# Optimization experiments

Measured on AMD Instinct MI355X. Metric: run time of the kernel, lower is better.

## Reference

```python
import jax, jax.numpy as jnp
import numpy as np

DIM = 1024
N_HEADS = 16
HEAD_DIM = DIM // N_HEADS
MAX_SEQ = 2048
BATCH = 4
SEQ = 2048


def _rope_tables(seq_len, head_dim):
    inv_freq = 1.0 / (10000.0 ** (jnp.arange(0, head_dim, 2, dtype=jnp.float32) / head_dim))
    t = jnp.arange(seq_len, dtype=jnp.float32)
    freqs = jnp.outer(t, inv_freq)            # [S, D/2]
    emb = jnp.concatenate([freqs, freqs], axis=-1)  # [S, D]
    return jnp.cos(emb), jnp.sin(emb)


def setup_inputs() -> dict:
    key = jax.random.key(0)
    kx, kq, kk, kv, ko = jax.random.split(key, 5)
    s = 1.0 / np.sqrt(DIM)
    x = jax.random.normal(kx, (BATCH, SEQ, DIM), dtype=jnp.float32)
    Wq = jax.random.normal(kq, (DIM, DIM), dtype=jnp.float32) * s
    Wk = jax.random.normal(kk, (DIM, DIM), dtype=jnp.float32) * s
    Wv = jax.random.normal(kv, (DIM, DIM), dtype=jnp.float32) * s
    Wo = jax.random.normal(ko, (DIM, DIM), dtype=jnp.float32) * s
    cos, sin = _rope_tables(SEQ, HEAD_DIM)
    mask = jnp.tril(jnp.ones((SEQ, SEQ), dtype=bool))[None, None]  # [1,1,S,S] causal
    return {"x": x, "Wq": Wq, "Wk": Wk, "Wv": Wv, "Wo": Wo,
            "cos": cos, "sin": sin, "mask": mask}


def _rotate_half(t):
    t1, t2 = jnp.split(t, 2, axis=-1)
    return jnp.concatenate([-t2, t1], axis=-1)


def reference(x, Wq, Wk, Wv, Wo, cos, sin, mask):
    B, S, _ = x.shape
    # projections (torch Linear: y = x @ W.T)
    q = (x @ Wq.T).reshape(B, S, N_HEADS, HEAD_DIM)
    k = (x @ Wk.T).reshape(B, S, N_HEADS, HEAD_DIM)
    v = (x @ Wv.T).reshape(B, S, N_HEADS, HEAD_DIM)
    # RoPE on [B,S,H,D]: cos/sin broadcast over batch and heads
    c = cos[None, :S, None, :]
    s_ = sin[None, :S, None, :]
    q = q * c + _rotate_half(q) * s_
    k = k * c + _rotate_half(k) * s_
    # attention, heads-major
    scale = HEAD_DIM ** -0.5
    attn = jnp.einsum('bqhd,bkhd->bhqk', q, k) * scale
    attn = jnp.where(mask, attn, -jnp.inf)
    attn = jax.nn.softmax(attn, axis=-1)
    out = jnp.einsum('bhqk,bkhd->bqhd', attn, v).reshape(B, S, DIM)
    return out @ Wo.T
```

## Files before the change

kernel.cpp:

```cpp
#include <hip/hip_runtime.h>
#include <hip/hip_bf16.h>
#include <stdint.h>

typedef __bf16 bf16;
typedef __bf16 bf16x4 __attribute__((ext_vector_type(4)));
typedef __bf16 bf16x8 __attribute__((ext_vector_type(8)));
typedef float f32x4 __attribute__((ext_vector_type(4)));

static constexpr int DIMM  = 1024;
static constexpr int NHEADS = 16;
static constexpr int HDIM  = 64;
static constexpr int SEQL  = 2048;
static constexpr int NB    = 4;
static constexpr int MTOT  = NB * SEQL;
static constexpr float LOG2E = 1.4426950408889634f;

__device__ __forceinline__ int swz(int row, int kc) {
    return row * 128 + ((kc ^ (row & 7)) << 4);
}

__device__ __forceinline__ void gl_lds16(const bf16* g, bf16* l) {
    __builtin_amdgcn_global_load_lds(
        (const __attribute__((address_space(1))) unsigned int*)g,
        (__attribute__((address_space(3))) unsigned int*)l,
        16, 0, 0);
}

__device__ __forceinline__ bf16x8 cvt8(f32x4 a, f32x4 b) {
    bf16x8 r;
    r[0] = (bf16)a[0]; r[1] = (bf16)a[1]; r[2] = (bf16)a[2]; r[3] = (bf16)a[3];
    r[4] = (bf16)b[0]; r[5] = (bf16)b[1]; r[6] = (bf16)b[2]; r[7] = (bf16)b[3];
    return r;
}

__global__ __launch_bounds__(256)
void cvt_kernel(const float* __restrict__ x,  const float* __restrict__ Wq,
                const float* __restrict__ Wk, const float* __restrict__ Wv,
                const float* __restrict__ Wo,
                bf16* __restrict__ xb,  bf16* __restrict__ Wqb,
                bf16* __restrict__ Wkb, bf16* __restrict__ Wvb,
                bf16* __restrict__ Wob)
{
    const size_t NX = (size_t)MTOT * DIMM;
    const size_t NW = (size_t)DIMM * DIMM;
    size_t i = ((size_t)blockIdx.x * 256 + threadIdx.x) * 8;
    const float* src; bf16* dst; size_t off;
    if (i < NX) { src = x; dst = xb; off = i; }
    else {
        size_t j = i - NX;
        int wsel = (int)(j >> 20);
        off = j & (NW - 1);
        if      (wsel == 0) { src = Wq; dst = Wqb; }
        else if (wsel == 1) { src = Wk; dst = Wkb; }
        else if (wsel == 2) { src = Wv; dst = Wvb; }
        else                { src = Wo; dst = Wob; }
    }
    f32x4 a = *(const f32x4*)(src + off);
    f32x4 b = *(const f32x4*)(src + off + 4);
    *(bf16x8*)(dst + off) = cvt8(a, b);
}

__global__ __launch_bounds__(256, 2)
void qkv_kernel(const bf16* __restrict__ xb,
                const bf16* __restrict__ Wqb, const bf16* __restrict__ Wkb,
                const bf16* __restrict__ Wvb,
                const float* __restrict__ cosT, const float* __restrict__ sinT,
                bf16* __restrict__ qb, bf16* __restrict__ kb, bf16* __restrict__ vTb)
{
    __shared__ __align__(16) bf16 As[2][128 * 32];
    __shared__ __align__(16) bf16 Bq[2][128 * 32];
    __shared__ __align__(16) bf16 Bk[2][128 * 32];
    __shared__ __align__(16) bf16 Bv[2][128 * 32];

    const int bid = (int)blockIdx.x;
    const int bn  = (bid & 7) * 128;
    const int bm  = (bid >> 3) * 128;

    const int tid  = threadIdx.x;
    const int lane = tid & 63;
    const int w    = tid >> 6;
    const int l15  = lane & 15;
    const int lg   = lane >> 4;
    const int wm   = (w >> 1) * 64;
    const int wn   = (w & 1) * 64;

    f32x4 acc[3][4][4];
    #pragma unroll
    for (int w3 = 0; w3 < 3; ++w3)
        #pragma unroll
        for (int mf = 0; mf < 4; ++mf)
            #pragma unroll
            for (int nf = 0; nf < 4; ++nf)
                acc[w3][mf][nf] = f32x4{0.f, 0.f, 0.f, 0.f};

    const int c0  = w * 2;
    const int rp0 = lane >> 3;
    const int tt  = (lane & 7) ^ rp0;
    const int rgo = (tt >> 2) << 6;
    const int kq  = (tt & 3) * 8;

    auto stage = [&](int t, int buf) {
        const int k0 = t * 32;
        #pragma unroll
        for (int i = 0; i < 2; ++i) {
            const int c  = c0 + i;
            const int rg = c * 8 + rp0 + rgo;
            const size_t am = (size_t)(bm + rg) * DIMM + k0 + kq;
            const size_t an = (size_t)(bn + rg) * DIMM + k0 + kq;
            gl_lds16(xb  + am, &As[buf][c * 512]);
            gl_lds16(Wqb + an, &Bq[buf][c * 512]);
            gl_lds16(Wkb + an, &Bk[buf][c * 512]);
            gl_lds16(Wvb + an, &Bv[buf][c * 512]);
        }
    };

    auto rd = [&](const bf16* base, int row) {
        return *(const bf16x8*)((const char*)base +
            (row & 63) * 128 + (((((row >> 6) << 2) | lg) ^ (row & 7)) << 4));
    };

    auto compute = [&](int buf) {
        bf16x8 af[4];
        #pragma unroll
        for (int mf = 0; mf < 4; ++mf)
            af[mf] = rd(As[buf], wm + mf * 16 + l15);
        const bf16* bsel[3] = {Bq[buf], Bk[buf], Bv[buf]};
        __builtin_amdgcn_s_setprio(1);
        #pragma unroll
        for (int w3 = 0; w3 < 3; ++w3) {
            bf16x8 bfr[4];
            #pragma unroll
            for (int nf = 0; nf < 4; ++nf)
                bfr[nf] = rd(bsel[w3], wn + nf * 16 + l15);
            #pragma unroll
            for (int mf = 0; mf < 4; ++mf)
                #pragma unroll
                for (int nf = 0; nf < 4; ++nf)
                    acc[w3][mf][nf] = __builtin_amdgcn_mfma_f32_16x16x32_bf16(
                        af[mf], bfr[nf], acc[w3][mf][nf], 0, 0, 0);
        }
        __builtin_amdgcn_s_setprio(0);
    };

    stage(0, 0);
    #pragma unroll 1
    for (int t = 0; t < 31; ++t) {
        stage(t + 1, (t + 1) & 1);
        asm volatile("s_waitcnt vmcnt(8)" ::: "memory");
        __builtin_amdgcn_s_barrier();
        __builtin_amdgcn_sched_barrier(0);
        compute(t & 1);
        __builtin_amdgcn_sched_barrier(0);
        __builtin_amdgcn_s_barrier();
    }
    asm volatile("s_waitcnt vmcnt(0)" ::: "memory");
    __builtin_amdgcn_s_barrier();
    __builtin_amdgcn_sched_barrier(0);
    compute(1);

    #pragma unroll
    for (int mf = 0; mf < 4; ++mf) {
        #pragma unroll
        for (int nf = 0; nf < 4; ++nf) {
            int n = bn + wn + nf * 16 + l15;
            int h = n >> 6;
            int d = n & 63;
            float sign = (d < 32) ? -1.f : 1.f;
            #pragma unroll
            for (int r = 0; r < 4; ++r) {
                int m = bm + wm + mf * 16 + lg * 4 + r;
                int b = m >> 11, s = m & 2047;
                float c  = cosT[s * 64 + d];
                float sv = sinT[s * 64 + d];
                size_t o_qk = ((size_t)((b * NHEADS + h) * SEQL + s)) * HDIM + d;
                float q0 = acc[0][mf][nf][r], q1 = acc[0][mf][nf ^ 2][r];
                float k0v = acc[1][mf][nf][r], k1 = acc[1][mf][nf ^ 2][r];
                qb[o_qk] = (bf16)((q0 * c + sign * q1 * sv) * (0.125f * LOG2E));
                kb[o_qk] = (bf16)(k0v * c + sign * k1 * sv);
                vTb[((size_t)((b * NHEADS + h) * HDIM + d)) * SEQL + s] = (bf16)acc[2][mf][nf][r];
            }
        }
    }
}

__global__ __launch_bounds__(256, 3)
void attn_kernel(bf16* __restrict__ qb, const bf16* __restrict__ kb,
                 const bf16* __restrict__ vTb)
{
    __shared__ __align__(16) bf16 Ks[2][64 * 64];
    __shared__ __align__(16) bf16 Vs[2][64 * 64];
    __shared__ __align__(16) bf16 Pl[4][32 * 64];

    const int bh  = blockIdx.x;
    const int qt  = 15 - (int)blockIdx.y;
    const int tid = threadIdx.x;
    const int lane = tid & 63, w = tid >> 6;
    const int l15 = lane & 15, lg = lane >> 4;

    bf16*       Qp = qb  + (size_t)bh * SEQL * HDIM;
    const bf16* Kp = kb  + (size_t)bh * SEQL * HDIM;
    const bf16* Vp = vTb + (size_t)bh * HDIM * SEQL;

    const int q0  = qt * 128 + w * 32;
    const int njt = 2 * qt + 2;

    bf16x8 qf[2][2];
    #pragma unroll
    for (int mf = 0; mf < 2; ++mf)
        #pragma unroll
        for (int ks = 0; ks < 2; ++ks)
            qf[mf][ks] = *(const bf16x8*)(Qp + (size_t)(q0 + mf * 16 + l15) * HDIM + ks * 32 + lg * 8);

    f32x4 oacc[4][2];
    float lsum[2] = {0.f, 0.f};
    #pragma unroll
    for (int nd = 0; nd < 4; ++nd)
        #pragma unroll
        for (int mf = 0; mf < 2; ++mf)
            oacc[nd][mf] = f32x4{0.f, 0.f, 0.f, 0.f};

    char* Pw = (char*)Pl[w];
    const int l7 = l15 & 7;
    const int srow0 = tid >> 3;
    const int skc   = tid & 7;

    bf16x8 kr[2], vr[2];
    auto issue = [&](int j) {
        const int kk0 = j * 64;
        #pragma unroll
        for (int c = 0; c < 2; ++c) {
            int row = c * 32 + srow0;
            kr[c] = *(const bf16x8*)(Kp + (size_t)(kk0 + row) * HDIM + skc * 8);
            vr[c] = *(const bf16x8*)(Vp + (size_t)row * SEQL + kk0 + skc * 8);
        }
    };
    auto commit = [&](int b) {
        #pragma unroll
        for (int c = 0; c < 2; ++c) {
            int row = c * 32 + srow0;
            *(bf16x8*)((char*)Ks[b] + swz(row, skc)) = kr[c];
            *(bf16x8*)((char*)Vs[b] + swz(row, skc)) = vr[c];
        }
    };

    issue(0);
    commit(0);
    __syncthreads();

    for (int j = 0; j < njt; ++j) {
        const int kk0 = j * 64;
        const int buf = j & 1;
        const bool more = (j + 1 < njt);
        if (more) issue(j + 1);

        f32x4 sacc[4][2];
        #pragma unroll
        for (int nf = 0; nf < 4; ++nf)
            #pragma unroll
            for (int mf = 0; mf < 2; ++mf)
                sacc[nf][mf] = f32x4{0.f, 0.f, 0.f, 0.f};
        #pragma unroll
        for (int ks = 0; ks < 2; ++ks) {
            bf16x8 kf[4];
            #pragma unroll
            for (int nf = 0; nf < 4; ++nf)
                kf[nf] = *(const bf16x8*)((const char*)Ks[buf] + swz(nf * 16 + l15, ks * 4 + lg));
            #pragma unroll
            for (int nf = 0; nf < 4; ++nf)
                #pragma unroll
                for (int mf = 0; mf < 2; ++mf)
                    sacc[nf][mf] = __builtin_amdgcn_mfma_f32_16x16x32_bf16(
                        kf[nf], qf[mf][ks], sacc[nf][mf], 0, 0, 0);
        }

        const bool nm = (kk0 + 63 > q0);
        #pragma unroll
        for (int nf = 0; nf < 4; ++nf) {
            #pragma unroll
            for (int mf = 0; mf < 2; ++mf) {
                float pv[4];
                #pragma unroll
                for (int r = 0; r < 4; ++r) {
                    float s = sacc[nf][mf][r];
                    if (nm) {
                        int kv = kk0 + nf * 16 + lg * 4 + r;
                        int qq = q0 + mf * 16 + l15;
                        if (kv > qq) s = -1.0e30f;
                    }
                    pv[r] = exp2f(s);
                }
                lsum[mf] += (pv[0] + pv[1]) + (pv[2] + pv[3]);
                bf16x4 pb;
                pb[0] = (bf16)pv[0]; pb[1] = (bf16)pv[1];
                pb[2] = (bf16)pv[2]; pb[3] = (bf16)pv[3];
                *(bf16x4*)(Pw + (mf * 16 + l15) * 128
                              + (((2 * nf + (lg >> 1)) ^ l7) << 4) + (lg & 1) * 8) = pb;
            }
        }

        #pragma unroll
        for (int ks = 0; ks < 2; ++ks) {
            bf16x8 pf[2], vf[4];
            #pragma unroll
            for (int mf = 0; mf < 2; ++mf)
                pf[mf] = *(const bf16x8*)(Pw + (mf * 16 + l15) * 128
                                             + (((ks * 4 + lg) ^ l7) << 4));
            #pragma unroll
            for (int nd = 0; nd < 4; ++nd)
                vf[nd] = *(const bf16x8*)((const char*)Vs[buf] + swz(nd * 16 + l15, ks * 4 + lg));
            #pragma unroll
            for (int nd = 0; nd < 4; ++nd)
                #pragma unroll
                for (int mf = 0; mf < 2; ++mf)
                    oacc[nd][mf] = __builtin_amdgcn_mfma_f32_16x16x32_bf16(
                        vf[nd], pf[mf], oacc[nd][mf], 0, 0, 0);
        }

        if (more) {
            commit(buf ^ 1);
            __syncthreads();
        }
    }

    #pragma unroll
    for (int mf = 0; mf < 2; ++mf) {
        lsum[mf] += __shfl_xor(lsum[mf], 16);
        lsum[mf] += __shfl_xor(lsum[mf], 32);
    }
    float inv[2] = {1.f / lsum[0], 1.f / lsum[1]};
    #pragma unroll
    for (int nd = 0; nd < 4; ++nd)
        #pragma unroll
        for (int mf = 0; mf < 2; ++mf) {
            bf16x4 o4;
            #pragma unroll
            for (int r = 0; r < 4; ++r)
                o4[r] = (bf16)(oacc[nd][mf][r] * inv[mf]);
            int s = q0 + mf * 16 + l15;
            int d = nd * 16 + lg * 4;
            *(bf16x4*)(Qp + (size_t)s * HDIM + d) = o4;
        }
}

__global__ __launch_bounds__(256, 2)
void oproj_kernel(const bf16* __restrict__ O, const bf16* __restrict__ Wob,
                  float* __restrict__ outp)
{
    __shared__ __align__(16) bf16 Bs[2][128 * 32];

    const int bm = (int)blockIdx.x * 128;
    const int bn = (int)blockIdx.y * 128;

    const int tid  = threadIdx.x;
    const int lane = tid & 63;
    const int w    = tid >> 6;
    const int l15  = lane & 15;
    const int lg   = lane >> 4;
    const int wm   = (w >> 1) * 64;
    const int wn   = (w & 1) * 64;

    f32x4 acc[4][4];
    #pragma unroll
    for (int mf = 0; mf < 4; ++mf)
        #pragma unroll
        for (int nf = 0; nf < 4; ++nf)
            acc[mf][nf] = f32x4{0.f, 0.f, 0.f, 0.f};

    const int c0  = w * 2;
    const int rp0 = lane >> 3;
    const int tt  = (lane & 7) ^ rp0;
    const int rgo = (tt >> 2) << 6;
    const int kq  = (tt & 3) * 8;

    auto stageB = [&](int t, int buf) {
        const int k0 = t * 32;
        #pragma unroll
        for (int i = 0; i < 2; ++i) {
            const int c  = c0 + i;
            const int rg = c * 8 + rp0 + rgo;
            gl_lds16(Wob + (size_t)(bn + rg) * DIMM + k0 + kq, &Bs[buf][c * 512]);
        }
    };

    auto loadA = [&](bf16x8 (&dst)[4], int t) {
        const int k0 = t * 32;
        #pragma unroll
        for (int mf = 0; mf < 4; ++mf) {
            int m = bm + wm + mf * 16 + l15;
            int b = m >> 11, s = m & 2047;
            int k = k0 + lg * 8;
            int h = k >> 6, dd = k & 63;
            dst[mf] = *(const bf16x8*)(O + ((size_t)((b * NHEADS + h) * SEQL + s)) * HDIM + dd);
        }
    };

    auto rd = [&](const bf16* base, int row) {
        return *(const bf16x8*)((const char*)base +
            (row & 63) * 128 + (((((row >> 6) << 2) | lg) ^ (row & 7)) << 4));
    };

    auto compute = [&](int buf, const bf16x8 (&af)[4]) {
        bf16x8 bfr[4];
        #pragma unroll
        for (int nf = 0; nf < 4; ++nf)
            bfr[nf] = rd(Bs[buf], wn + nf * 16 + l15);
        #pragma unroll
        for (int mf = 0; mf < 4; ++mf)
            #pragma unroll
            for (int nf = 0; nf < 4; ++nf)
                acc[mf][nf] = __builtin_amdgcn_mfma_f32_16x16x32_bf16(
                    af[mf], bfr[nf], acc[mf][nf], 0, 0, 0);
    };

    bf16x8 aA[4], aB[4];

    stageB(0, 0);
    __builtin_amdgcn_sched_barrier(0);
    loadA(aA, 0);
    __builtin_amdgcn_sched_barrier(0);

    auto step = [&](bf16x8 (&cur)[4], bf16x8 (&nxt)[4], int t) {
        stageB(t + 1, (t + 1) & 1);
        __builtin_amdgcn_sched_barrier(0);
        asm volatile("s_waitcnt vmcnt(6)" ::: "memory");
        __builtin_amdgcn_s_barrier();
        __builtin_amdgcn_sched_barrier(0);
        loadA(nxt, t + 1);
        compute(t & 1, cur);
        __builtin_amdgcn_sched_barrier(0);
        __builtin_amdgcn_s_barrier();
    };

    #pragma unroll 1
    for (int tp = 0; tp < 15; ++tp) {
        step(aA, aB, 2 * tp);
        step(aB, aA, 2 * tp + 1);
    }
    step(aA, aB, 30);
    asm volatile("s_waitcnt vmcnt(0)" ::: "memory");
    __builtin_amdgcn_s_barrier();
    __builtin_amdgcn_sched_barrier(0);
    compute(1, aB);

    #pragma unroll
    for (int mf = 0; mf < 4; ++mf)
        #pragma unroll
        for (int nf = 0; nf < 4; ++nf) {
            int n = bn + wn + nf * 16 + l15;
            #pragma unroll
            for (int r = 0; r < 4; ++r) {
                int m = bm + wm + mf * 16 + lg * 4 + r;
                outp[(size_t)m * DIMM + n] = acc[mf][nf][r];
            }
        }
}

extern "C" void kernel_launch(void* const* d_in, const int* in_sizes, int n_in,
                              void* d_out, int out_size, void* d_ws, size_t ws_size,
                              hipStream_t stream)
{
    const float* x    = (const float*)d_in[0];
    const float* Wq   = (const float*)d_in[1];
    const float* Wk   = (const float*)d_in[2];
    const float* Wv   = (const float*)d_in[3];
    const float* Wo   = (const float*)d_in[4];
    const float* cosT = (const float*)d_in[5];
    const float* sinT = (const float*)d_in[6];

    const size_t NELEM = (size_t)MTOT * DIMM;
    const size_t NW    = (size_t)DIMM * DIMM;
    bf16* qb  = (bf16*)d_ws;
    bf16* kb  = qb + NELEM;
    bf16* vT  = kb + NELEM;
    bf16* xb  = vT + NELEM;
    bf16* Wqb = xb + NELEM;
    bf16* Wkb = Wqb + NW;
    bf16* Wvb = Wkb + NW;
    bf16* Wob = Wvb + NW;

    dim3 blk(256);
    cvt_kernel<<<dim3(6144), blk, 0, stream>>>(x, Wq, Wk, Wv, Wo,
                                               xb, Wqb, Wkb, Wvb, Wob);

    qkv_kernel<<<dim3(512), blk, 0, stream>>>(xb, Wqb, Wkb, Wvb, cosT, sinT,
                                              qb, kb, vT);

    dim3 g2(NB * NHEADS, SEQL / 128);
    attn_kernel<<<g2, blk, 0, stream>>>(qb, kb, vT);

    dim3 g3(MTOT / 128, DIMM / 128);
    oproj_kernel<<<g3, blk, 0, stream>>>(qb, Wob, (float*)d_out);
}
```

Measured before the change: 176.2 us.

## Fuse x fp32-to-bf16 conversion into QKV GEMM and compute softmax row sums via MFMA

The separate conversion pass over x is removed. The QKV kernel now streams fp32 x tiles directly into LDS and converts them to bf16 when it loads fragments, which avoids writing and re-reading a bf16 copy of x. In exchange the A tile in LDS doubles in size and global reads of x in the GEMM double, which raises LDS use and may cut occupancy. Separately, the attention kernel computes the softmax denominator with an extra MFMA against a ones vector instead of scalar adds plus cross-lane shuffles, so the sum is now taken over bf16-rounded probabilities.

```diff
diff --git a/kernel.cpp b/kernel.cpp
--- a/kernel.cpp
+++ b/kernel.cpp
@@ -19,7 +19,7 @@
     return row * 128 + ((kc ^ (row & 7)) << 4);
 }
 
-__device__ __forceinline__ void gl_lds16(const bf16* g, bf16* l) {
+__device__ __forceinline__ void gl_lds16(const void* g, void* l) {
     __builtin_amdgcn_global_load_lds(
         (const __attribute__((address_space(1))) unsigned int*)g,
         (__attribute__((address_space(3))) unsigned int*)l,
@@ -34,43 +34,36 @@
 }
 
 __global__ __launch_bounds__(256)
-void cvt_kernel(const float* __restrict__ x,  const float* __restrict__ Wq,
-                const float* __restrict__ Wk, const float* __restrict__ Wv,
-                const float* __restrict__ Wo,
-                bf16* __restrict__ xb,  bf16* __restrict__ Wqb,
-                bf16* __restrict__ Wkb, bf16* __restrict__ Wvb,
-                bf16* __restrict__ Wob)
+void cvt_kernel(const float* __restrict__ Wq, const float* __restrict__ Wk,
+                const float* __restrict__ Wv, const float* __restrict__ Wo,
+                bf16* __restrict__ Wqb, bf16* __restrict__ Wkb,
+                bf16* __restrict__ Wvb, bf16* __restrict__ Wob)
 {
-    const size_t NX = (size_t)MTOT * DIMM;
     const size_t NW = (size_t)DIMM * DIMM;
     size_t i = ((size_t)blockIdx.x * 256 + threadIdx.x) * 8;
-    const float* src; bf16* dst; size_t off;
-    if (i < NX) { src = x; dst = xb; off = i; }
-    else {
-        size_t j = i - NX;
-        int wsel = (int)(j >> 20);
-        off = j & (NW - 1);
-        if      (wsel == 0) { src = Wq; dst = Wqb; }
-        else if (wsel == 1) { src = Wk; dst = Wkb; }
-        else if (wsel == 2) { src = Wv; dst = Wvb; }
-        else                { src = Wo; dst = Wob; }
-    }
+    int wsel = (int)(i >> 20);
+    size_t off = i & (NW - 1);
+    const float* src; bf16* dst;
+    if      (wsel == 0) { src = Wq; dst = Wqb; }
+    else if (wsel == 1) { src = Wk; dst = Wkb; }
+    else if (wsel == 2) { src = Wv; dst = Wvb; }
+    else                { src = Wo; dst = Wob; }
     f32x4 a = *(const f32x4*)(src + off);
     f32x4 b = *(const f32x4*)(src + off + 4);
     *(bf16x8*)(dst + off) = cvt8(a, b);
 }
 
 __global__ __launch_bounds__(256, 2)
-void qkv_kernel(const bf16* __restrict__ xb,
+void qkv_kernel(const float* __restrict__ xf,
                 const bf16* __restrict__ Wqb, const bf16* __restrict__ Wkb,
                 const bf16* __restrict__ Wvb,
                 const float* __restrict__ cosT, const float* __restrict__ sinT,
                 bf16* __restrict__ qb, bf16* __restrict__ kb, bf16* __restrict__ vTb)
 {
-    __shared__ __align__(16) bf16 As[2][128 * 32];
-    __shared__ __align__(16) bf16 Bq[2][128 * 32];
-    __shared__ __align__(16) bf16 Bk[2][128 * 32];
-    __shared__ __align__(16) bf16 Bv[2][128 * 32];
+    __shared__ __align__(16) float AsF[2][128 * 32];
+    __shared__ __align__(16) bf16  Bq[2][128 * 32];
+    __shared__ __align__(16) bf16  Bk[2][128 * 32];
+    __shared__ __align__(16) bf16  Bv[2][128 * 32];
 
     const int bid = (int)blockIdx.x;
     const int bn  = (bid & 7) * 128;
@@ -81,6 +74,7 @@
     const int w    = tid >> 6;
     const int l15  = lane & 15;
     const int lg   = lane >> 4;
+    const int l7   = l15 & 7;
     const int wm   = (w >> 1) * 64;
     const int wn   = (w & 1) * 64;
 
@@ -95,26 +89,33 @@
 
     const int c0  = w * 2;
     const int rp0 = lane >> 3;
-    const int tt  = (lane & 7) ^ rp0;
-    const int rgo = (tt >> 2) << 6;
-    const int kq  = (tt & 3) * 8;
+    const int ttb = (lane & 7) ^ rp0;
+    const int rgo = (ttb >> 2) << 6;
+    const int kqb = (ttb & 3) * 8;
+
+    const int ca0 = w * 4;
+    const int kqa = ((lane & 7) ^ rp0) * 4;
 
     auto stage = [&](int t, int buf) {
         const int k0 = t * 32;
+        #pragma unroll
+        for (int i = 0; i < 4; ++i) {
+            const int c = ca0 + i;
+            gl_lds16(xf + (size_t)(bm + c * 8 + rp0) * DIMM + k0 + kqa,
+                     &AsF[buf][c * 256]);
+        }
         #pragma unroll
         for (int i = 0; i < 2; ++i) {
             const int c  = c0 + i;
             const int rg = c * 8 + rp0 + rgo;
-            const size_t am = (size_t)(bm + rg) * DIMM + k0 + kq;
-            const size_t an = (size_t)(bn + rg) * DIMM + k0 + kq;
-            gl_lds16(xb  + am, &As[buf][c * 512]);
+            const size_t an = (size_t)(bn + rg) * DIMM + k0 + kqb;
             gl_lds16(Wqb + an, &Bq[buf][c * 512]);
             gl_lds16(Wkb + an, &Bk[buf][c * 512]);
             gl_lds16(Wvb + an, &Bv[buf][c * 512]);
         }
     };
 
-    auto rd = [&](const bf16* base, int row) {
+    auto rdB = [&](const bf16* base, int row) {
         return *(const bf16x8*)((const char*)base +
             (row & 63) * 128 + (((((row >> 6) << 2) | lg) ^ (row & 7)) << 4));
     };
@@ -122,8 +123,13 @@
     auto compute = [&](int buf) {
         bf16x8 af[4];
         #pragma unroll
-        for (int mf = 0; mf < 4; ++mf)
-            af[mf] = rd(As[buf], wm + mf * 16 + l15);
+        for (int mf = 0; mf < 4; ++mf) {
+            const int row = wm + mf * 16 + l15;
+            const char* rb = (const char*)AsF[buf] + row * 128;
+            f32x4 a0 = *(const f32x4*)(rb + (((2 * lg    ) ^ l7) << 4));
+            f32x4 a1 = *(const f32x4*)(rb + (((2 * lg + 1) ^ l7) << 4));
+            af[mf] = cvt8(a0, a1);
+        }
         const bf16* bsel[3] = {Bq[buf], Bk[buf], Bv[buf]};
         __builtin_amdgcn_s_setprio(1);
         #pragma unroll
@@ -131,7 +137,7 @@
             bf16x8 bfr[4];
             #pragma unroll
             for (int nf = 0; nf < 4; ++nf)
-                bfr[nf] = rd(bsel[w3], wn + nf * 16 + l15);
+                bfr[nf] = rdB(bsel[w3], wn + nf * 16 + l15);
             #pragma unroll
             for (int mf = 0; mf < 4; ++mf)
                 #pragma unroll
@@ -146,7 +152,7 @@
     #pragma unroll 1
     for (int t = 0; t < 31; ++t) {
         stage(t + 1, (t + 1) & 1);
-        asm volatile("s_waitcnt vmcnt(8)" ::: "memory");
+        asm volatile("s_waitcnt vmcnt(10)" ::: "memory");
         __builtin_amdgcn_s_barrier();
         __builtin_amdgcn_sched_barrier(0);
         compute(t & 1);
@@ -211,8 +217,14 @@
         for (int ks = 0; ks < 2; ++ks)
             qf[mf][ks] = *(const bf16x8*)(Qp + (size_t)(q0 + mf * 16 + l15) * HDIM + ks * 32 + lg * 8);
 
+    bf16x8 ones;
+    #pragma unroll
+    for (int e = 0; e < 8; ++e) ones[e] = (bf16)1.0f;
+
     f32x4 oacc[4][2];
-    float lsum[2] = {0.f, 0.f};
+    f32x4 lacc[2];
+    #pragma unroll
+    for (int mf = 0; mf < 2; ++mf) lacc[mf] = f32x4{0.f, 0.f, 0.f, 0.f};
     #pragma unroll
     for (int nd = 0; nd < 4; ++nd)
         #pragma unroll
@@ -278,7 +290,7 @@
         for (int nf = 0; nf < 4; ++nf) {
             #pragma unroll
             for (int mf = 0; mf < 2; ++mf) {
-                float pv[4];
+                bf16x4 pb;
                 #pragma unroll
                 for (int r = 0; r < 4; ++r) {
                     float s = sacc[nf][mf][r];
@@ -287,12 +299,8 @@
                         int qq = q0 + mf * 16 + l15;
                         if (kv > qq) s = -1.0e30f;
                     }
-                    pv[r] = exp2f(s);
+                    pb[r] = (bf16)exp2f(s);
                 }
-                lsum[mf] += (pv[0] + pv[1]) + (pv[2] + pv[3]);
-                bf16x4 pb;
-                pb[0] = (bf16)pv[0]; pb[1] = (bf16)pv[1];
-                pb[2] = (bf16)pv[2]; pb[3] = (bf16)pv[3];
                 *(bf16x4*)(Pw + (mf * 16 + l15) * 128
                               + (((2 * nf + (lg >> 1)) ^ l7) << 4) + (lg & 1) * 8) = pb;
             }
@@ -308,6 +316,10 @@
             #pragma unroll
             for (int nd = 0; nd < 4; ++nd)
                 vf[nd] = *(const bf16x8*)((const char*)Vs[buf] + swz(nd * 16 + l15, ks * 4 + lg));
+            #pragma unroll
+            for (int mf = 0; mf < 2; ++mf)
+                lacc[mf] = __builtin_amdgcn_mfma_f32_16x16x32_bf16(
+                    ones, pf[mf], lacc[mf], 0, 0, 0);
             #pragma unroll
             for (int nd = 0; nd < 4; ++nd)
                 #pragma unroll
@@ -322,12 +334,7 @@
         }
     }
 
-    #pragma unroll
-    for (int mf = 0; mf < 2; ++mf) {
-        lsum[mf] += __shfl_xor(lsum[mf], 16);
-        lsum[mf] += __shfl_xor(lsum[mf], 32);
-    }
-    float inv[2] = {1.f / lsum[0], 1.f / lsum[1]};
+    float inv[2] = {1.f / lacc[0][0], 1.f / lacc[1][0]};
     #pragma unroll
     for (int nd = 0; nd < 4; ++nd)
         #pragma unroll
@@ -472,17 +479,15 @@
     bf16* qb  = (bf16*)d_ws;
     bf16* kb  = qb + NELEM;
     bf16* vT  = kb + NELEM;
-    bf16* xb  = vT + NELEM;
-    bf16* Wqb = xb + NELEM;
+    bf16* Wqb = vT + NELEM;
     bf16* Wkb = Wqb + NW;
     bf16* Wvb = Wkb + NW;
     bf16* Wob = Wvb + NW;
 
     dim3 blk(256);
-    cvt_kernel<<<dim3(6144), blk, 0, stream>>>(x, Wq, Wk, Wv, Wo,
-                                               xb, Wqb, Wkb, Wvb, Wob);
-
-    qkv_kernel<<<dim3(512), blk, 0, stream>>>(xb, Wqb, Wkb, Wvb, cosT, sinT,
+    cvt_kernel<<<dim3(2048), blk, 0, stream>>>(Wq, Wk, Wv, Wo, Wqb, Wkb, Wvb, Wob);
+
+    qkv_kernel<<<dim3(512), blk, 0, stream>>>(x, Wqb, Wkb, Wvb, cosT, sinT,
                                               qb, kb, vT);
 
     dim3 g2(NB * NHEADS, SEQL / 128);
```

New measurement: 190.7 us. 1.08x slower.
